# Optimization experiments

Hardware: AMD Instinct MI355X
Metric: run time of the kernel (lower is better)

## Reference

```python
import math
import jax, jax.numpy as jnp
import numpy as np

B, T, C, HS = 8, 2048, 1024, 64

def setup_inputs() -> dict:
    key = jax.random.key(0)
    kx, kq, kk, kv = jax.random.split(key, 4)
    x = jax.random.normal(kx, (B, T, C), dtype=jnp.float32)
    # match nn.Linear init scale roughly: U(-1/sqrt(C), 1/sqrt(C))
    lim = 1.0 / math.sqrt(C)
    Wq = jax.random.uniform(kq, (C, HS), minval=-lim, maxval=lim, dtype=jnp.float32)
    Wk = jax.random.uniform(kk, (C, HS), minval=-lim, maxval=lim, dtype=jnp.float32)
    Wv = jax.random.uniform(kv, (C, HS), minval=-lim, maxval=lim, dtype=jnp.float32)
    return {"x": x, "Wq": Wq, "Wk": Wk, "Wv": Wv}

def reference(x, Wq, Wk, Wv):
    # NOTE: original scales by 1/sqrt(hs) where hs = x.shape[-1] = embd_size,
    # not head_size. Faithfully reproduced.
    Tlen = x.shape[1]
    scale = 1.0 / math.sqrt(x.shape[-1])
    q = jnp.einsum('btc,ch->bth', x, Wq)
    k = jnp.einsum('btc,ch->bth', x, Wk)
    v = jnp.einsum('btc,ch->bth', x, Wv)
    wei = jnp.einsum('bth,bsh->bts', q, k) * scale  # [B,T,T]
    causal = jnp.tril(jnp.ones((Tlen, Tlen), dtype=bool))
    wei = jnp.where(causal, wei, -jnp.inf)
    wei = jax.nn.softmax(wei, axis=-1)
    # dropout p=0.0 -> identity
    out = jnp.einsum('bts,bsh->bth', wei, v)  # [B,T,HS]
    return out
```

## Files before the change

### kernel.cpp

```cpp
#include <hip/hip_runtime.h>
#include <hip/hip_bf16.h>


#define T_SEQ 2048
#define C_DIM 1024
#define HS 64
#define BT 16384

typedef short s8v __attribute__((ext_vector_type(8)));
typedef float f4v __attribute__((ext_vector_type(4)));

__device__ inline unsigned short f2bf(float f) {
  union { float f; unsigned u; } a; a.f = f;
  unsigned r = a.u + 0x7fffu + ((a.u >> 16) & 1u);
  return (unsigned short)(r >> 16);
}

__device__ inline unsigned pk2(float a, float b) {
  union { __hip_bfloat162 h; unsigned u; } c;
  c.h = __float22bfloat162_rn(make_float2(a, b));
  return c.u;
}

__device__ inline s8v cvt8(float4 v0, float4 v1) {
  union { unsigned u[4]; s8v v; } r;
  r.u[0] = pk2(v0.x, v0.y); r.u[1] = pk2(v0.z, v0.w);
  r.u[2] = pk2(v1.x, v1.y); r.u[3] = pk2(v1.z, v1.w);
  return r.v;
}

__device__ inline void gl_lds16(const void* g, unsigned char* lds_base,
                                unsigned uniform_byte_off) {
  __builtin_amdgcn_global_load_lds(
      (const __attribute__((address_space(1))) unsigned int*)g,
      (__attribute__((address_space(3))) unsigned int*)(lds_base + uniform_byte_off),
      16, 0, 0);
}

__global__ __launch_bounds__(256) void wt_kernel(
    const float* __restrict__ Wq, const float* __restrict__ Wk,
    const float* __restrict__ Wv, unsigned short* __restrict__ wt) {
  __shared__ float tile[64][65];
  const int bid = blockIdx.x;
  const int mat = bid >> 4, kt = bid & 15;
  const float* W = (mat == 0) ? Wq : ((mat == 1) ? Wk : Wv);
  const int t = threadIdx.x;
  const int n = t & 63, kr = t >> 6;
#pragma unroll
  for (int j = 0; j < 16; ++j) {
    const int kl = j * 4 + kr;
    tile[kl][n] = W[(kt * 64 + kl) * HS + n];
  }
  __syncthreads();
  const int n2 = t >> 2, kp = t & 3;
  unsigned int* orow =
      (unsigned int*)(wt + (size_t)(mat * 64 + n2) * C_DIM + kt * 64);
#pragma unroll
  for (int i = 0; i < 8; ++i) {
    const int k0 = kp * 16 + i * 2;
    unsigned int lo = f2bf(tile[k0][n2]);
    unsigned int hi = f2bf(tile[k0 + 1][n2]);
    orow[kp * 8 + i] = lo | (hi << 16);
  }
}

__global__ __launch_bounds__(256) void qkv_kernel(
    const float* __restrict__ x, const unsigned short* __restrict__ wt,
    unsigned short* __restrict__ qws, unsigned short* __restrict__ kws,
    unsigned short* __restrict__ vtws) {
  __shared__ unsigned char abuf[2][8192];
  __shared__ unsigned char bbuf[2][24576];

  const int tid  = threadIdx.x;
  const int wv   = tid >> 6;
  const int lane = tid & 63;
  const int m    = lane & 15;
  const int quad = lane >> 4;
  const int row0 = blockIdx.x * 32;
  const int mh   = wv >> 1;
  const int ng   = (wv & 1) * 6;

  f4v acc[6];
#pragma unroll
  for (int j = 0; j < 6; ++j) acc[j] = (f4v)0.0f;

  const unsigned au = (unsigned)__builtin_amdgcn_readfirstlane(tid & 192) << 4;

  const float* agp[2];
#pragma unroll
  for (int j = 0; j < 2; ++j) {
    const int s = tid + j * 256;
    const int r = s >> 4, p = (s & 15) ^ (r & 15);
    agp[j] = x + (size_t)(row0 + r) * C_DIM + p * 4;
  }
  const unsigned short* bgp[6];
#pragma unroll
  for (int j = 0; j < 6; ++j) {
    const int s = tid + j * 256;
    const int n = s >> 3, p = (s & 7) ^ (n & 7);
    bgp[j] = wt + (size_t)n * C_DIM + p * 8;
  }

  int aoff[2][2];
#pragma unroll
  for (int c = 0; c < 2; ++c)
#pragma unroll
    for (int t = 0; t < 2; ++t)
      aoff[c][t] = (((mh * 16 + m) * 16) + ((c * 8 + 2 * quad + t) ^ m)) << 4;
  int boff[6][2];
#pragma unroll
  for (int j = 0; j < 6; ++j) {
    const int n = (ng + j) * 16 + m;
#pragma unroll
    for (int c = 0; c < 2; ++c)
      boff[j][c] = (n * 8 + ((c * 4 + quad) ^ (n & 7))) << 4;
  }

#define STAGE(buf, kk)                                                       \
  do {                                                                       \
    _Pragma("unroll") for (int j = 0; j < 2; ++j)                            \
        gl_lds16(agp[j] + (kk), abuf[buf], au + (unsigned)(j * 4096));       \
    _Pragma("unroll") for (int j = 0; j < 6; ++j)                            \
        gl_lds16(bgp[j] + (kk), bbuf[buf], au + (unsigned)(j * 4096));       \
  } while (0)

  STAGE(0, 0);
  for (int it = 0; it < 16; ++it) {
    __syncthreads();
    if (it < 15) STAGE((it + 1) & 1, (it + 1) * 64);
    const unsigned char* aB = abuf[it & 1];
    const unsigned char* bB = bbuf[it & 1];
#pragma unroll
    for (int c = 0; c < 2; ++c) {
      float4 xa = *(const float4*)(aB + aoff[c][0]);
      float4 xb = *(const float4*)(aB + aoff[c][1]);
      s8v a = cvt8(xa, xb);
#pragma unroll
      for (int j = 0; j < 6; ++j) {
        s8v b = *(const s8v*)(bB + boff[j][c]);
        acc[j] = __builtin_amdgcn_mfma_f32_16x16x32_bf16(a, b, acc[j], 0, 0, 0);
      }
    }
  }
#undef STAGE

  const float qscale = 1.4426950408889634f / 32.0f;
#pragma unroll
  for (int j = 0; j < 6; ++j) {
    const int nt = ng + j;
    const int mat = nt >> 2, ct = nt & 3;
    const int col = ct * 16 + m;
#pragma unroll
    for (int r = 0; r < 4; ++r) {
      const int row = row0 + mh * 16 + quad * 4 + r;
      const float v = acc[j][r];
      if (mat == 0) {
        qws[row * HS + col] = f2bf(v * qscale);
      } else if (mat == 1) {
        kws[row * HS + col] = f2bf(v);
      } else {
        const int bb = row >> 11, t = row & 2047;
        const int tp = (t & ~63) | (((t & 15) << 2) | ((t >> 4) & 3));
        vtws[(bb * HS + col) * T_SEQ + tp] = f2bf(v);
      }
    }
  }
}

union __align__(16) AttnSh {
  unsigned short p[8][4][16 * 72];
  float mo[8][32][64];
};

__global__ __launch_bounds__(512) void attn_kernel(
    const unsigned short* __restrict__ qws, const unsigned short* __restrict__ kws,
    const unsigned short* __restrict__ vtws, float* __restrict__ out) {
  __shared__ AttnSh sh;
  __shared__ float ml[8][32];

  const int tid  = threadIdx.x;
  const int wv   = tid >> 6;
  const int lane = tid & 63;
  const int m    = lane & 15;
  const int quad = lane >> 4;
  const int b    = blockIdx.x & 7;
  const int pr   = blockIdx.x >> 3;
  const int rS   = pr * 32;
  const int rB   = (63 - pr) * 32;
  const int grS  = b * T_SEQ + rS;
  const int grB  = b * T_SEQ + rB;

  const unsigned short* qpS = qws + (size_t)(grS + m) * HS + quad * 8;
  const unsigned short* qpB = qws + (size_t)(grB + m) * HS + quad * 8;
  s8v aq[4][2];
  aq[0][0] = *(const s8v*)qpS;
  aq[0][1] = *(const s8v*)(qpS + 32);
  aq[1][0] = *(const s8v*)(qpS + 16 * HS);
  aq[1][1] = *(const s8v*)(qpS + 16 * HS + 32);
  aq[2][0] = *(const s8v*)qpB;
  aq[2][1] = *(const s8v*)(qpB + 32);
  aq[3][0] = *(const s8v*)(qpB + 16 * HS);
  aq[3][1] = *(const s8v*)(qpB + 16 * HS + 32);

  float li[4][4];
  f4v o[4][4];
#pragma unroll
  for (int t = 0; t < 4; ++t)
#pragma unroll
    for (int i = 0; i < 4; ++i) { li[t][i] = 0.f; o[t][i] = (f4v)0.0f; }

  const int nstS = (rS + 32 + 63) >> 6;
  const int nstB = (rB + 32 + 63) >> 6;
  const int qb0 = rS + quad * 4;
  const int qb1 = qb0 + 16;
  const int qb2 = rB + quad * 4;
  const int qb3 = qb2 + 16;
  const unsigned short* kbase = kws + (size_t)b * T_SEQ * HS;
  const unsigned short* vbase = vtws + (size_t)b * HS * T_SEQ;

#define QKT(t, qbase)                                                        \
  {                                                                          \
    f4v s_[4];                                                               \
    _Pragma("unroll") for (int ns = 0; ns < 4; ++ns) {                       \
      f4v u_ = (f4v)0.0f;                                                    \
      u_ = __builtin_amdgcn_mfma_f32_16x16x32_bf16(aq[t][0], kf[ns][0], u_, 0, 0, 0); \
      u_ = __builtin_amdgcn_mfma_f32_16x16x32_bf16(aq[t][1], kf[ns][1], u_, 0, 0, 0); \
      s_[ns] = u_;                                                           \
    }                                                                        \
    _Pragma("unroll") for (int r = 0; r < 4; ++r) {                          \
      const int qr = (qbase) + r;                                            \
      const float p0 = (sm      > qr) ? 0.f : __builtin_amdgcn_exp2f(s_[0][r]); \
      const float p1 = (sm + 16 > qr) ? 0.f : __builtin_amdgcn_exp2f(s_[1][r]); \
      const float p2 = (sm + 32 > qr) ? 0.f : __builtin_amdgcn_exp2f(s_[2][r]); \
      const float p3 = (sm + 48 > qr) ? 0.f : __builtin_amdgcn_exp2f(s_[3][r]); \
      li[t][r] += (p0 + p1) + (p2 + p3);                                     \
      *(uint2*)&sh.p[wv][t][(quad * 4 + r) * 72 + m * 4] =                   \
          make_uint2(pk2(p0, p1), pk2(p2, p3));                              \
    }                                                                        \
  }

#define PVT(t)                                                               \
  {                                                                          \
    const unsigned short* pl_ = sh.p[wv][t];                                 \
    s8v a0_ = *(const s8v*)&pl_[m * 72 + quad * 8];                          \
    s8v a1_ = *(const s8v*)&pl_[m * 72 + 32 + quad * 8];                     \
    _Pragma("unroll") for (int hn = 0; hn < 4; ++hn) {                       \
      o[t][hn] = __builtin_amdgcn_mfma_f32_16x16x32_bf16(a0_, vf[hn][0], o[t][hn], 0, 0, 0); \
      o[t][hn] = __builtin_amdgcn_mfma_f32_16x16x32_bf16(a1_, vf[hn][1], o[t][hn], 0, 0, 0); \
    }                                                                        \
  }

  for (int st = wv; st < nstB; st += 8) {
    const int s0 = st * 64;

    s8v kf[4][2];
#pragma unroll
    for (int ns = 0; ns < 4; ++ns) {
      const unsigned short* kp = &kbase[(size_t)(s0 + ns * 16 + m) * HS + quad * 8];
      kf[ns][0] = *(const s8v*)kp;
      kf[ns][1] = *(const s8v*)(kp + 32);
    }
    s8v vf[4][2];
#pragma unroll
    for (int hn = 0; hn < 4; ++hn) {
      const unsigned short* vp = &vbase[(size_t)(hn * 16 + m) * T_SEQ + s0 + quad * 8];
      vf[hn][0] = *(const s8v*)vp;
      vf[hn][1] = *(const s8v*)(vp + 32);
    }

    const int sm = s0 + m;
    const bool low = (st < nstS);
    if (low) { QKT(0, qb0); QKT(1, qb1); }
    QKT(2, qb2);
    QKT(3, qb3);
    if (low) { PVT(0); PVT(1); }
    PVT(2);
    PVT(3);
  }
#undef QKT
#undef PVT

#pragma unroll
  for (int t = 0; t < 4; ++t)
#pragma unroll
    for (int r = 0; r < 4; ++r) {
      float s = li[t][r];
      s += __shfl_xor(s, 1); s += __shfl_xor(s, 2);
      s += __shfl_xor(s, 4); s += __shfl_xor(s, 8);
      li[t][r] = s;
    }

  const int row = tid >> 4, c4 = (tid & 15) * 4;
#pragma unroll
  for (int ps = 0; ps < 2; ++ps) {
    __syncthreads();
#pragma unroll
    for (int hn = 0; hn < 4; ++hn)
#pragma unroll
      for (int r = 0; r < 4; ++r) {
        sh.mo[wv][quad * 4 + r][hn * 16 + m]      = o[2 * ps][hn][r];
        sh.mo[wv][16 + quad * 4 + r][hn * 16 + m] = o[2 * ps + 1][hn][r];
      }
    if (m == 0) {
#pragma unroll
      for (int r = 0; r < 4; ++r) {
        ml[wv][quad * 4 + r]      = li[2 * ps][r];
        ml[wv][16 + quad * 4 + r] = li[2 * ps + 1][r];
      }
    }
    __syncthreads();

    float ls = 0.f;
#pragma unroll
    for (int w = 0; w < 8; ++w) ls += ml[w][row];
    const float inv = 1.0f / ls;
    float ax = 0.f, ay = 0.f, az = 0.f, aw = 0.f;
#pragma unroll
    for (int w = 0; w < 8; ++w) {
      float4 v = *(const float4*)&sh.mo[w][row][c4];
      ax += v.x; ay += v.y; az += v.z; aw += v.w;
    }
    const int gr = ps ? grB : grS;
    float4 res;
    res.x = ax * inv; res.y = ay * inv; res.z = az * inv; res.w = aw * inv;
    *(float4*)&out[(size_t)(gr + row) * HS + c4] = res;
  }
}

extern "C" void kernel_launch(void* const* d_in, const int* in_sizes, int n_in,
                              void* d_out, int out_size, void* d_ws, size_t ws_size,
                              hipStream_t stream) {
  const float* x  = (const float*)d_in[0];
  const float* Wq = (const float*)d_in[1];
  const float* Wk = (const float*)d_in[2];
  const float* Wv = (const float*)d_in[3];
  float* out = (float*)d_out;

  unsigned short* qws  = (unsigned short*)d_ws;
  unsigned short* kws  = qws + (size_t)BT * HS;
  unsigned short* vtws = kws + (size_t)BT * HS;
  unsigned short* wt   = vtws + (size_t)BT * HS;

  wt_kernel<<<dim3(48), dim3(256), 0, stream>>>(Wq, Wk, Wv, wt);
  qkv_kernel<<<dim3(BT / 32), dim3(256), 0, stream>>>(x, wt, qws, kws, vtws);
  attn_kernel<<<dim3(256), dim3(512), 0, stream>>>(qws, kws, vtws, out);
}
```

Measured before the change: 135.4 us.

## Fuse weight transpose, QKV projection and attention into one cooperative kernel

Replaces the three separate launches (weight transpose/convert, QKV projection, attention) with a single cooperative kernel of 256 blocks that uses grid-wide syncs between the phases. The QKV phase is retiled to 64 rows per 512-thread block so the same grid shape serves every phase. The aim is to remove two kernel launch gaps and their tail drain. In exchange it adds grid.sync and threadfence overhead and a larger shared-memory union, and the QKV phase now runs only 256 blocks instead of 512.

```diff
diff --git a/kernel.cpp b/kernel.cpp
--- a/kernel.cpp
+++ b/kernel.cpp
@@ -1,5 +1,8 @@
 #include <hip/hip_runtime.h>
 #include <hip/hip_bf16.h>
+#include <hip/hip_cooperative_groups.h>
+
+namespace cg = cooperative_groups;
 
 
 #define T_SEQ 2048
@@ -37,186 +40,187 @@
       16, 0, 0);
 }
 
-__global__ __launch_bounds__(256) void wt_kernel(
-    const float* __restrict__ Wq, const float* __restrict__ Wk,
-    const float* __restrict__ Wv, unsigned short* __restrict__ wt) {
-  __shared__ float tile[64][65];
-  const int bid = blockIdx.x;
-  const int mat = bid >> 4, kt = bid & 15;
-  const float* W = (mat == 0) ? Wq : ((mat == 1) ? Wk : Wv);
-  const int t = threadIdx.x;
-  const int n = t & 63, kr = t >> 6;
-#pragma unroll
-  for (int j = 0; j < 16; ++j) {
-    const int kl = j * 4 + kr;
-    tile[kl][n] = W[(kt * 64 + kl) * HS + n];
-  }
-  __syncthreads();
-  const int n2 = t >> 2, kp = t & 3;
-  unsigned int* orow =
-      (unsigned int*)(wt + (size_t)(mat * 64 + n2) * C_DIM + kt * 64);
-#pragma unroll
-  for (int i = 0; i < 8; ++i) {
-    const int k0 = kp * 16 + i * 2;
-    unsigned int lo = f2bf(tile[k0][n2]);
-    unsigned int hi = f2bf(tile[k0 + 1][n2]);
-    orow[kp * 8 + i] = lo | (hi << 16);
-  }
-}
-
-__global__ __launch_bounds__(256) void qkv_kernel(
-    const float* __restrict__ x, const unsigned short* __restrict__ wt,
-    unsigned short* __restrict__ qws, unsigned short* __restrict__ kws,
-    unsigned short* __restrict__ vtws) {
-  __shared__ unsigned char abuf[2][8192];
-  __shared__ unsigned char bbuf[2][24576];
+union __align__(16) FusedSh {
+  struct { unsigned char a[2][16384]; unsigned char b[2][24576]; } qk;
+  struct { unsigned short p[8][4][16 * 72]; } at;
+  struct { float mo[8][32][64]; } mg;
+  float wtile[64][65];
+};
+
+__global__ __launch_bounds__(512, 2) void fused_kernel(
+    const float* __restrict__ x, const float* __restrict__ Wq,
+    const float* __restrict__ Wk, const float* __restrict__ Wv,
+    unsigned short* __restrict__ wt, unsigned short* __restrict__ qws,
+    unsigned short* __restrict__ kws, unsigned short* __restrict__ vtws,
+    float* __restrict__ out) {
+  __shared__ FusedSh sh;
+  __shared__ float ml[8][32];
+
+  cg::grid_group grid = cg::this_grid();
 
   const int tid  = threadIdx.x;
+  const int bid  = blockIdx.x;
   const int wv   = tid >> 6;
   const int lane = tid & 63;
   const int m    = lane & 15;
   const int quad = lane >> 4;
-  const int row0 = blockIdx.x * 32;
-  const int mh   = wv >> 1;
-  const int ng   = (wv & 1) * 6;
-
-  f4v acc[6];
-#pragma unroll
-  for (int j = 0; j < 6; ++j) acc[j] = (f4v)0.0f;
-
-  const unsigned au = (unsigned)__builtin_amdgcn_readfirstlane(tid & 192) << 4;
-
-  const float* agp[2];
-#pragma unroll
-  for (int j = 0; j < 2; ++j) {
-    const int s = tid + j * 256;
-    const int r = s >> 4, p = (s & 15) ^ (r & 15);
-    agp[j] = x + (size_t)(row0 + r) * C_DIM + p * 4;
-  }
-  const unsigned short* bgp[6];
-#pragma unroll
-  for (int j = 0; j < 6; ++j) {
-    const int s = tid + j * 256;
-    const int n = s >> 3, p = (s & 7) ^ (n & 7);
-    bgp[j] = wt + (size_t)n * C_DIM + p * 8;
-  }
-
-  int aoff[2][2];
-#pragma unroll
-  for (int c = 0; c < 2; ++c)
-#pragma unroll
-    for (int t = 0; t < 2; ++t)
-      aoff[c][t] = (((mh * 16 + m) * 16) + ((c * 8 + 2 * quad + t) ^ m)) << 4;
-  int boff[6][2];
-#pragma unroll
-  for (int j = 0; j < 6; ++j) {
-    const int n = (ng + j) * 16 + m;
+
+  if (bid < 48) {
+    const int mat = bid >> 4, kt = bid & 15;
+    const float* W = (mat == 0) ? Wq : ((mat == 1) ? Wk : Wv);
+    const int n = tid & 63, kr = tid >> 6;
+#pragma unroll
+    for (int j = 0; j < 8; ++j) {
+      const int kl = j * 8 + kr;
+      sh.wtile[kl][n] = W[(kt * 64 + kl) * HS + n];
+    }
+    __syncthreads();
+    const int n2 = tid >> 3, kp = tid & 7;
+    unsigned int* orow =
+        (unsigned int*)(wt + (size_t)(mat * 64 + n2) * C_DIM + kt * 64);
+#pragma unroll
+    for (int i = 0; i < 4; ++i) {
+      const int k0 = kp * 8 + i * 2;
+      unsigned lo = f2bf(sh.wtile[k0][n2]);
+      unsigned hi = f2bf(sh.wtile[k0 + 1][n2]);
+      orow[kp * 4 + i] = lo | (hi << 16);
+    }
+  }
+  __threadfence();
+  grid.sync();
+  __threadfence();
+
+  {
+    const int wq = wv & 3, th = wv >> 2;
+    const int mh = wq >> 1, ng = (wq & 1) * 6;
+    const int row0 = bid * 64;
+
+    f4v acc[6];
+#pragma unroll
+    for (int j = 0; j < 6; ++j) acc[j] = (f4v)0.0f;
+
+    const unsigned au = (unsigned)__builtin_amdgcn_readfirstlane(tid & 448) << 4;
+
+    const float* agp[2];
+#pragma unroll
+    for (int j = 0; j < 2; ++j) {
+      const int s = tid + j * 512;
+      const int r = s >> 4, p = (s & 15) ^ (r & 15);
+      agp[j] = x + (size_t)(row0 + r) * C_DIM + p * 4;
+    }
+    const unsigned short* bgp[3];
+#pragma unroll
+    for (int j = 0; j < 3; ++j) {
+      const int s = tid + j * 512;
+      const int n = s >> 3, p = (s & 7) ^ (n & 7);
+      bgp[j] = wt + (size_t)n * C_DIM + p * 8;
+    }
+
+    int aoff[2][2];
 #pragma unroll
     for (int c = 0; c < 2; ++c)
-      boff[j][c] = (n * 8 + ((c * 4 + quad) ^ (n & 7))) << 4;
-  }
+#pragma unroll
+      for (int t = 0; t < 2; ++t)
+        aoff[c][t] =
+            (((th * 32 + mh * 16 + m) * 16) + ((c * 8 + 2 * quad + t) ^ m)) << 4;
+    int boff[6][2];
+#pragma unroll
+    for (int j = 0; j < 6; ++j) {
+      const int n = (ng + j) * 16 + m;
+#pragma unroll
+      for (int c = 0; c < 2; ++c)
+        boff[j][c] = (n * 8 + ((c * 4 + quad) ^ (n & 7))) << 4;
+    }
 
 #define STAGE(buf, kk)                                                       \
   do {                                                                       \
     _Pragma("unroll") for (int j = 0; j < 2; ++j)                            \
-        gl_lds16(agp[j] + (kk), abuf[buf], au + (unsigned)(j * 4096));       \
-    _Pragma("unroll") for (int j = 0; j < 6; ++j)                            \
-        gl_lds16(bgp[j] + (kk), bbuf[buf], au + (unsigned)(j * 4096));       \
+        gl_lds16(agp[j] + (kk), sh.qk.a[buf], au + (unsigned)(j * 8192));    \
+    _Pragma("unroll") for (int j = 0; j < 3; ++j)                            \
+        gl_lds16(bgp[j] + (kk), sh.qk.b[buf], au + (unsigned)(j * 8192));    \
   } while (0)
 
-  STAGE(0, 0);
-  for (int it = 0; it < 16; ++it) {
-    __syncthreads();
-    if (it < 15) STAGE((it + 1) & 1, (it + 1) * 64);
-    const unsigned char* aB = abuf[it & 1];
-    const unsigned char* bB = bbuf[it & 1];
-#pragma unroll
-    for (int c = 0; c < 2; ++c) {
-      float4 xa = *(const float4*)(aB + aoff[c][0]);
-      float4 xb = *(const float4*)(aB + aoff[c][1]);
-      s8v a = cvt8(xa, xb);
-#pragma unroll
-      for (int j = 0; j < 6; ++j) {
-        s8v b = *(const s8v*)(bB + boff[j][c]);
-        acc[j] = __builtin_amdgcn_mfma_f32_16x16x32_bf16(a, b, acc[j], 0, 0, 0);
-      }
-    }
-  }
+    STAGE(0, 0);
+    for (int it = 0; it < 16; ++it) {
+      __syncthreads();
+      if (it < 15) STAGE((it + 1) & 1, (it + 1) * 64);
+      const unsigned char* aB = sh.qk.a[it & 1];
+      const unsigned char* bB = sh.qk.b[it & 1];
+#pragma unroll
+      for (int c = 0; c < 2; ++c) {
+        float4 xa = *(const float4*)(aB + aoff[c][0]);
+        float4 xb = *(const float4*)(aB + aoff[c][1]);
+        s8v a = cvt8(xa, xb);
+#pragma unroll
+        for (int j = 0; j < 6; ++j) {
+          s8v b = *(const s8v*)(bB + boff[j][c]);
+          acc[j] = __builtin_amdgcn_mfma_f32_16x16x32_bf16(a, b, acc[j], 0, 0, 0);
+        }
+      }
+    }
 #undef STAGE
 
-  const float qscale = 1.4426950408889634f / 32.0f;
-#pragma unroll
-  for (int j = 0; j < 6; ++j) {
-    const int nt = ng + j;
-    const int mat = nt >> 2, ct = nt & 3;
-    const int col = ct * 16 + m;
-#pragma unroll
-    for (int r = 0; r < 4; ++r) {
-      const int row = row0 + mh * 16 + quad * 4 + r;
-      const float v = acc[j][r];
-      if (mat == 0) {
-        qws[row * HS + col] = f2bf(v * qscale);
-      } else if (mat == 1) {
-        kws[row * HS + col] = f2bf(v);
-      } else {
-        const int bb = row >> 11, t = row & 2047;
-        const int tp = (t & ~63) | (((t & 15) << 2) | ((t >> 4) & 3));
-        vtws[(bb * HS + col) * T_SEQ + tp] = f2bf(v);
-      }
-    }
-  }
-}
-
-union __align__(16) AttnSh {
-  unsigned short p[8][4][16 * 72];
-  float mo[8][32][64];
-};
-
-__global__ __launch_bounds__(512) void attn_kernel(
-    const unsigned short* __restrict__ qws, const unsigned short* __restrict__ kws,
-    const unsigned short* __restrict__ vtws, float* __restrict__ out) {
-  __shared__ AttnSh sh;
-  __shared__ float ml[8][32];
-
-  const int tid  = threadIdx.x;
-  const int wv   = tid >> 6;
-  const int lane = tid & 63;
-  const int m    = lane & 15;
-  const int quad = lane >> 4;
-  const int b    = blockIdx.x & 7;
-  const int pr   = blockIdx.x >> 3;
-  const int rS   = pr * 32;
-  const int rB   = (63 - pr) * 32;
-  const int grS  = b * T_SEQ + rS;
-  const int grB  = b * T_SEQ + rB;
-
-  const unsigned short* qpS = qws + (size_t)(grS + m) * HS + quad * 8;
-  const unsigned short* qpB = qws + (size_t)(grB + m) * HS + quad * 8;
-  s8v aq[4][2];
-  aq[0][0] = *(const s8v*)qpS;
-  aq[0][1] = *(const s8v*)(qpS + 32);
-  aq[1][0] = *(const s8v*)(qpS + 16 * HS);
-  aq[1][1] = *(const s8v*)(qpS + 16 * HS + 32);
-  aq[2][0] = *(const s8v*)qpB;
-  aq[2][1] = *(const s8v*)(qpB + 32);
-  aq[3][0] = *(const s8v*)(qpB + 16 * HS);
-  aq[3][1] = *(const s8v*)(qpB + 16 * HS + 32);
-
-  float li[4][4];
-  f4v o[4][4];
-#pragma unroll
-  for (int t = 0; t < 4; ++t)
-#pragma unroll
-    for (int i = 0; i < 4; ++i) { li[t][i] = 0.f; o[t][i] = (f4v)0.0f; }
-
-  const int nstS = (rS + 32 + 63) >> 6;
-  const int nstB = (rB + 32 + 63) >> 6;
-  const int qb0 = rS + quad * 4;
-  const int qb1 = qb0 + 16;
-  const int qb2 = rB + quad * 4;
-  const int qb3 = qb2 + 16;
-  const unsigned short* kbase = kws + (size_t)b * T_SEQ * HS;
-  const unsigned short* vbase = vtws + (size_t)b * HS * T_SEQ;
+    const float qscale = 1.4426950408889634f / 32.0f;
+#pragma unroll
+    for (int j = 0; j < 6; ++j) {
+      const int nt = ng + j;
+      const int mat = nt >> 2, ct = nt & 3;
+      const int col = ct * 16 + m;
+#pragma unroll
+      for (int r = 0; r < 4; ++r) {
+        const int row = row0 + th * 32 + mh * 16 + quad * 4 + r;
+        const float v = acc[j][r];
+        if (mat == 0) {
+          qws[row * HS + col] = f2bf(v * qscale);
+        } else if (mat == 1) {
+          kws[row * HS + col] = f2bf(v);
+        } else {
+          const int bb = row >> 11, t = row & 2047;
+          const int tp = (t & ~63) | (((t & 15) << 2) | ((t >> 4) & 3));
+          vtws[(bb * HS + col) * T_SEQ + tp] = f2bf(v);
+        }
+      }
+    }
+  }
+  __threadfence();
+  grid.sync();
+  __threadfence();
+
+  {
+    const int b  = bid & 7;
+    const int pr = bid >> 3;
+    const int rS = pr * 32;
+    const int rB = (63 - pr) * 32;
+    const int grS = b * T_SEQ + rS;
+    const int grB = b * T_SEQ + rB;
+
+    const unsigned short* qpS = qws + (size_t)(grS + m) * HS + quad * 8;
+    const unsigned short* qpB = qws + (size_t)(grB + m) * HS + quad * 8;
+    s8v aq[4][2];
+    aq[0][0] = *(const s8v*)qpS;
+    aq[0][1] = *(const s8v*)(qpS + 32);
+    aq[1][0] = *(const s8v*)(qpS + 16 * HS);
+    aq[1][1] = *(const s8v*)(qpS + 16 * HS + 32);
+    aq[2][0] = *(const s8v*)qpB;
+    aq[2][1] = *(const s8v*)(qpB + 32);
+    aq[3][0] = *(const s8v*)(qpB + 16 * HS);
+    aq[3][1] = *(const s8v*)(qpB + 16 * HS + 32);
+
+    float li[4][4];
+    f4v o[4][4];
+#pragma unroll
+    for (int t = 0; t < 4; ++t)
+#pragma unroll
+      for (int i = 0; i < 4; ++i) { li[t][i] = 0.f; o[t][i] = (f4v)0.0f; }
+
+    const int nstS = (rS + 32 + 63) >> 6;
+    const int nstB = (rB + 32 + 63) >> 6;
+    const int qb0 = rS + quad * 4;
+    const int qb1 = qb0 + 16;
+    const int qb2 = rB + quad * 4;
+    const int qb3 = qb2 + 16;
+    const unsigned short* kbase = kws + (size_t)b * T_SEQ * HS;
+    const unsigned short* vbase = vtws + (size_t)b * HS * T_SEQ;
 
 #define QKT(t, qbase)                                                        \
   {                                                                          \
@@ -234,14 +238,14 @@
       const float p2 = (sm + 32 > qr) ? 0.f : __builtin_amdgcn_exp2f(s_[2][r]); \
       const float p3 = (sm + 48 > qr) ? 0.f : __builtin_amdgcn_exp2f(s_[3][r]); \
       li[t][r] += (p0 + p1) + (p2 + p3);                                     \
-      *(uint2*)&sh.p[wv][t][(quad * 4 + r) * 72 + m * 4] =                   \
+      *(uint2*)&sh.at.p[wv][t][(quad * 4 + r) * 72 + m * 4] =                \
           make_uint2(pk2(p0, p1), pk2(p2, p3));                              \
     }                                                                        \
   }
 
 #define PVT(t)                                                               \
   {                                                                          \
-    const unsigned short* pl_ = sh.p[wv][t];                                 \
+    const unsigned short* pl_ = sh.at.p[wv][t];                              \
     s8v a0_ = *(const s8v*)&pl_[m * 72 + quad * 8];                          \
     s8v a1_ = *(const s8v*)&pl_[m * 72 + 32 + quad * 8];                     \
     _Pragma("unroll") for (int hn = 0; hn < 4; ++hn) {                       \
@@ -250,80 +254,81 @@
     }                                                                        \
   }
 
-  for (int st = wv; st < nstB; st += 8) {
-    const int s0 = st * 64;
-
-    s8v kf[4][2];
-#pragma unroll
-    for (int ns = 0; ns < 4; ++ns) {
-      const unsigned short* kp = &kbase[(size_t)(s0 + ns * 16 + m) * HS + quad * 8];
-      kf[ns][0] = *(const s8v*)kp;
-      kf[ns][1] = *(const s8v*)(kp + 32);
-    }
-    s8v vf[4][2];
-#pragma unroll
-    for (int hn = 0; hn < 4; ++hn) {
-      const unsigned short* vp = &vbase[(size_t)(hn * 16 + m) * T_SEQ + s0 + quad * 8];
-      vf[hn][0] = *(const s8v*)vp;
-      vf[hn][1] = *(const s8v*)(vp + 32);
-    }
-
-    const int sm = s0 + m;
-    const bool low = (st < nstS);
-    if (low) { QKT(0, qb0); QKT(1, qb1); }
-    QKT(2, qb2);
-    QKT(3, qb3);
-    if (low) { PVT(0); PVT(1); }
-    PVT(2);
-    PVT(3);
-  }
+    for (int st = wv; st < nstB; st += 8) {
+      const int s0 = st * 64;
+
+      s8v kf[4][2];
+#pragma unroll
+      for (int ns = 0; ns < 4; ++ns) {
+        const unsigned short* kp = &kbase[(size_t)(s0 + ns * 16 + m) * HS + quad * 8];
+        kf[ns][0] = *(const s8v*)kp;
+        kf[ns][1] = *(const s8v*)(kp + 32);
+      }
+      s8v vf[4][2];
+#pragma unroll
+      for (int hn = 0; hn < 4; ++hn) {
+        const unsigned short* vp = &vbase[(size_t)(hn * 16 + m) * T_SEQ + s0 + quad * 8];
+        vf[hn][0] = *(const s8v*)vp;
+        vf[hn][1] = *(const s8v*)(vp + 32);
+      }
+
+      const int sm = s0 + m;
+      const bool low = (st < nstS);
+      if (low) { QKT(0, qb0); QKT(1, qb1); }
+      QKT(2, qb2);
+      QKT(3, qb3);
+      if (low) { PVT(0); PVT(1); }
+      PVT(2);
+      PVT(3);
+    }
 #undef QKT
 #undef PVT
 
 #pragma unroll
-  for (int t = 0; t < 4; ++t)
-#pragma unroll
-    for (int r = 0; r < 4; ++r) {
-      float s = li[t][r];
-      s += __shfl_xor(s, 1); s += __shfl_xor(s, 2);
-      s += __shfl_xor(s, 4); s += __shfl_xor(s, 8);
-      li[t][r] = s;
-    }
-
-  const int row = tid >> 4, c4 = (tid & 15) * 4;
-#pragma unroll
-  for (int ps = 0; ps < 2; ++ps) {
-    __syncthreads();
-#pragma unroll
-    for (int hn = 0; hn < 4; ++hn)
+    for (int t = 0; t < 4; ++t)
 #pragma unroll
       for (int r = 0; r < 4; ++r) {
-        sh.mo[wv][quad * 4 + r][hn * 16 + m]      = o[2 * ps][hn][r];
-        sh.mo[wv][16 + quad * 4 + r][hn * 16 + m] = o[2 * ps + 1][hn][r];
-      }
-    if (m == 0) {
-#pragma unroll
-      for (int r = 0; r < 4; ++r) {
-        ml[wv][quad * 4 + r]      = li[2 * ps][r];
-        ml[wv][16 + quad * 4 + r] = li[2 * ps + 1][r];
-      }
-    }
-    __syncthreads();
-
-    float ls = 0.f;
-#pragma unroll
-    for (int w = 0; w < 8; ++w) ls += ml[w][row];
-    const float inv = 1.0f / ls;
-    float ax = 0.f, ay = 0.f, az = 0.f, aw = 0.f;
-#pragma unroll
-    for (int w = 0; w < 8; ++w) {
-      float4 v = *(const float4*)&sh.mo[w][row][c4];
-      ax += v.x; ay += v.y; az += v.z; aw += v.w;
-    }
-    const int gr = ps ? grB : grS;
-    float4 res;
-    res.x = ax * inv; res.y = ay * inv; res.z = az * inv; res.w = aw * inv;
-    *(float4*)&out[(size_t)(gr + row) * HS + c4] = res;
+        float s = li[t][r];
+        s += __shfl_xor(s, 1); s += __shfl_xor(s, 2);
+        s += __shfl_xor(s, 4); s += __shfl_xor(s, 8);
+        li[t][r] = s;
+      }
+
+    const int row = tid >> 4, c4 = (tid & 15) * 4;
+#pragma unroll
+    for (int ps = 0; ps < 2; ++ps) {
+      __syncthreads();
+#pragma unroll
+      for (int hn = 0; hn < 4; ++hn)
+#pragma unroll
+        for (int r = 0; r < 4; ++r) {
+          sh.mg.mo[wv][quad * 4 + r][hn * 16 + m]      = o[2 * ps][hn][r];
+          sh.mg.mo[wv][16 + quad * 4 + r][hn * 16 + m] = o[2 * ps + 1][hn][r];
+        }
+      if (m == 0) {
+#pragma unroll
+        for (int r = 0; r < 4; ++r) {
+          ml[wv][quad * 4 + r]      = li[2 * ps][r];
+          ml[wv][16 + quad * 4 + r] = li[2 * ps + 1][r];
+        }
+      }
+      __syncthreads();
+
+      float ls = 0.f;
+#pragma unroll
+      for (int w = 0; w < 8; ++w) ls += ml[w][row];
+      const float inv = 1.0f / ls;
+      float ax = 0.f, ay = 0.f, az = 0.f, aw = 0.f;
+#pragma unroll
+      for (int w = 0; w < 8; ++w) {
+        float4 v = *(const float4*)&sh.mg.mo[w][row][c4];
+        ax += v.x; ay += v.y; az += v.z; aw += v.w;
+      }
+      const int gr = ps ? grB : grS;
+      float4 res;
+      res.x = ax * inv; res.y = ay * inv; res.z = az * inv; res.w = aw * inv;
+      *(float4*)&out[(size_t)(gr + row) * HS + c4] = res;
+    }
   }
 }
 
@@ -341,7 +346,9 @@
   unsigned short* vtws = kws + (size_t)BT * HS;
   unsigned short* wt   = vtws + (size_t)BT * HS;
 
-  wt_kernel<<<dim3(48), dim3(256), 0, stream>>>(Wq, Wk, Wv, wt);
-  qkv_kernel<<<dim3(BT / 32), dim3(256), 0, stream>>>(x, wt, qws, kws, vtws);
-  attn_kernel<<<dim3(256), dim3(512), 0, stream>>>(qws, kws, vtws, out);
-}
+  void* args[] = {(void*)&x, (void*)&Wq, (void*)&Wk, (void*)&Wv,
+                  (void*)&wt, (void*)&qws, (void*)&kws, (void*)&vtws,
+                  (void*)&out};
+  hipLaunchCooperativeKernel((void*)fused_kernel, dim3(256), dim3(512),
+                             args, 0, stream);
+}
```

Result: slower. 388.8 us (+187.1%).

## Keep softmax probabilities in registers via transposed QK^T and grow QKV tiles

Applied to the files above, without the earlier changes.

The attention kernel now computes S^T by swapping the MFMA operands, so each lane holds probabilities along the key dimension. It packs them straight into bf16 A-operands for the PV MFMA, which removes the LDS round-trip for P, and the V workspace permutation is changed to match the new key ordering. Row sums now need only two cross-quad shuffles. Separately, the QKV projection block grows to 64 rows with 512 threads, so each weight tile staged in LDS is shared by twice as many rows, at the cost of more LDS per block and fewer resident blocks.

```diff
diff --git a/kernel.cpp b/kernel.cpp
--- a/kernel.cpp
+++ b/kernel.cpp
@@ -64,11 +64,11 @@
   }
 }
 
-__global__ __launch_bounds__(256) void qkv_kernel(
+__global__ __launch_bounds__(512) void qkv_kernel(
     const float* __restrict__ x, const unsigned short* __restrict__ wt,
     unsigned short* __restrict__ qws, unsigned short* __restrict__ kws,
     unsigned short* __restrict__ vtws) {
-  __shared__ unsigned char abuf[2][8192];
+  __shared__ unsigned char abuf[2][16384];
   __shared__ unsigned char bbuf[2][24576];
 
   const int tid  = threadIdx.x;
@@ -76,27 +76,27 @@
   const int lane = tid & 63;
   const int m    = lane & 15;
   const int quad = lane >> 4;
-  const int row0 = blockIdx.x * 32;
-  const int mh   = wv >> 1;
-  const int ng   = (wv & 1) * 6;
+  const int wq = wv & 3, th = wv >> 2;
+  const int mh = wq >> 1, ng = (wq & 1) * 6;
+  const int row0 = blockIdx.x * 64;
 
   f4v acc[6];
 #pragma unroll
   for (int j = 0; j < 6; ++j) acc[j] = (f4v)0.0f;
 
-  const unsigned au = (unsigned)__builtin_amdgcn_readfirstlane(tid & 192) << 4;
+  const unsigned au = (unsigned)__builtin_amdgcn_readfirstlane(tid & 448) << 4;
 
   const float* agp[2];
 #pragma unroll
   for (int j = 0; j < 2; ++j) {
-    const int s = tid + j * 256;
+    const int s = tid + j * 512;
     const int r = s >> 4, p = (s & 15) ^ (r & 15);
     agp[j] = x + (size_t)(row0 + r) * C_DIM + p * 4;
   }
-  const unsigned short* bgp[6];
-#pragma unroll
-  for (int j = 0; j < 6; ++j) {
-    const int s = tid + j * 256;
+  const unsigned short* bgp[3];
+#pragma unroll
+  for (int j = 0; j < 3; ++j) {
+    const int s = tid + j * 512;
     const int n = s >> 3, p = (s & 7) ^ (n & 7);
     bgp[j] = wt + (size_t)n * C_DIM + p * 8;
   }
@@ -106,7 +106,8 @@
   for (int c = 0; c < 2; ++c)
 #pragma unroll
     for (int t = 0; t < 2; ++t)
-      aoff[c][t] = (((mh * 16 + m) * 16) + ((c * 8 + 2 * quad + t) ^ m)) << 4;
+      aoff[c][t] =
+          (((th * 32 + mh * 16 + m) * 16) + ((c * 8 + 2 * quad + t) ^ m)) << 4;
   int boff[6][2];
 #pragma unroll
   for (int j = 0; j < 6; ++j) {
@@ -119,9 +120,9 @@
 #define STAGE(buf, kk)                                                       \
   do {                                                                       \
     _Pragma("unroll") for (int j = 0; j < 2; ++j)                            \
-        gl_lds16(agp[j] + (kk), abuf[buf], au + (unsigned)(j * 4096));       \
-    _Pragma("unroll") for (int j = 0; j < 6; ++j)                            \
-        gl_lds16(bgp[j] + (kk), bbuf[buf], au + (unsigned)(j * 4096));       \
+        gl_lds16(agp[j] + (kk), abuf[buf], au + (unsigned)(j * 8192));       \
+    _Pragma("unroll") for (int j = 0; j < 3; ++j)                            \
+        gl_lds16(bgp[j] + (kk), bbuf[buf], au + (unsigned)(j * 8192));       \
   } while (0)
 
   STAGE(0, 0);
@@ -152,7 +153,7 @@
     const int col = ct * 16 + m;
 #pragma unroll
     for (int r = 0; r < 4; ++r) {
-      const int row = row0 + mh * 16 + quad * 4 + r;
+      const int row = row0 + th * 32 + mh * 16 + quad * 4 + r;
       const float v = acc[j][r];
       if (mat == 0) {
         qws[row * HS + col] = f2bf(v * qscale);
@@ -160,22 +161,18 @@
         kws[row * HS + col] = f2bf(v);
       } else {
         const int bb = row >> 11, t = row & 2047;
-        const int tp = (t & ~63) | (((t & 15) << 2) | ((t >> 4) & 3));
-        vtws[(bb * HS + col) * T_SEQ + tp] = f2bf(v);
+        const int s = t & 63;
+        const int jp = (s & 32) | ((s & 12) << 1) | ((s & 16) >> 2) | (s & 3);
+        vtws[(bb * HS + col) * T_SEQ + ((t & ~63) | jp)] = f2bf(v);
       }
     }
   }
 }
-
-union __align__(16) AttnSh {
-  unsigned short p[8][4][16 * 72];
-  float mo[8][32][64];
-};
 
 __global__ __launch_bounds__(512) void attn_kernel(
     const unsigned short* __restrict__ qws, const unsigned short* __restrict__ kws,
     const unsigned short* __restrict__ vtws, float* __restrict__ out) {
-  __shared__ AttnSh sh;
+  __shared__ float mo[8][32][64];
   __shared__ float ml[8][32];
 
   const int tid  = threadIdx.x;
@@ -202,51 +199,50 @@
   aq[3][0] = *(const s8v*)(qpB + 16 * HS);
   aq[3][1] = *(const s8v*)(qpB + 16 * HS + 32);
 
-  float li[4][4];
+  float li[4] = {0.f, 0.f, 0.f, 0.f};
   f4v o[4][4];
 #pragma unroll
   for (int t = 0; t < 4; ++t)
 #pragma unroll
-    for (int i = 0; i < 4; ++i) { li[t][i] = 0.f; o[t][i] = (f4v)0.0f; }
+    for (int i = 0; i < 4; ++i) o[t][i] = (f4v)0.0f;
 
   const int nstS = (rS + 32 + 63) >> 6;
   const int nstB = (rB + 32 + 63) >> 6;
-  const int qb0 = rS + quad * 4;
-  const int qb1 = qb0 + 16;
-  const int qb2 = rB + quad * 4;
-  const int qb3 = qb2 + 16;
+  const int qb0 = rS;
+  const int qb1 = rS + 16;
+  const int qb2 = rB;
+  const int qb3 = rB + 16;
   const unsigned short* kbase = kws + (size_t)b * T_SEQ * HS;
   const unsigned short* vbase = vtws + (size_t)b * HS * T_SEQ;
 
-#define QKT(t, qbase)                                                        \
+#define TILE(t, qb)                                                          \
   {                                                                          \
     f4v s_[4];                                                               \
     _Pragma("unroll") for (int ns = 0; ns < 4; ++ns) {                       \
       f4v u_ = (f4v)0.0f;                                                    \
-      u_ = __builtin_amdgcn_mfma_f32_16x16x32_bf16(aq[t][0], kf[ns][0], u_, 0, 0, 0); \
-      u_ = __builtin_amdgcn_mfma_f32_16x16x32_bf16(aq[t][1], kf[ns][1], u_, 0, 0, 0); \
+      u_ = __builtin_amdgcn_mfma_f32_16x16x32_bf16(kf[ns][0], aq[t][0], u_, 0, 0, 0); \
+      u_ = __builtin_amdgcn_mfma_f32_16x16x32_bf16(kf[ns][1], aq[t][1], u_, 0, 0, 0); \
       s_[ns] = u_;                                                           \
     }                                                                        \
-    _Pragma("unroll") for (int r = 0; r < 4; ++r) {                          \
-      const int qr = (qbase) + r;                                            \
-      const float p0 = (sm      > qr) ? 0.f : __builtin_amdgcn_exp2f(s_[0][r]); \
-      const float p1 = (sm + 16 > qr) ? 0.f : __builtin_amdgcn_exp2f(s_[1][r]); \
-      const float p2 = (sm + 32 > qr) ? 0.f : __builtin_amdgcn_exp2f(s_[2][r]); \
-      const float p3 = (sm + 48 > qr) ? 0.f : __builtin_amdgcn_exp2f(s_[3][r]); \
-      li[t][r] += (p0 + p1) + (p2 + p3);                                     \
-      *(uint2*)&sh.p[wv][t][(quad * 4 + r) * 72 + m * 4] =                   \
-          make_uint2(pk2(p0, p1), pk2(p2, p3));                              \
+    const int qr_ = (qb) + m;                                                \
+    union { unsigned u[4]; s8v v; } paA_, paB_;                              \
+    _Pragma("unroll") for (int ns = 0; ns < 4; ++ns) {                       \
+      const int sb_ = s0 + ns * 16 + quad * 4;                               \
+      const float p0 = (sb_     > qr_) ? 0.f : __builtin_amdgcn_exp2f(s_[ns][0]); \
+      const float p1 = (sb_ + 1 > qr_) ? 0.f : __builtin_amdgcn_exp2f(s_[ns][1]); \
+      const float p2 = (sb_ + 2 > qr_) ? 0.f : __builtin_amdgcn_exp2f(s_[ns][2]); \
+      const float p3 = (sb_ + 3 > qr_) ? 0.f : __builtin_amdgcn_exp2f(s_[ns][3]); \
+      li[t] += (p0 + p1) + (p2 + p3);                                        \
+      if (ns < 2) {                                                          \
+        paA_.u[ns * 2] = pk2(p0, p1); paA_.u[ns * 2 + 1] = pk2(p2, p3);      \
+      } else {                                                               \
+        paB_.u[(ns - 2) * 2] = pk2(p0, p1);                                  \
+        paB_.u[(ns - 2) * 2 + 1] = pk2(p2, p3);                              \
+      }                                                                      \
     }                                                                        \
-  }
-
-#define PVT(t)                                                               \
-  {                                                                          \
-    const unsigned short* pl_ = sh.p[wv][t];                                 \
-    s8v a0_ = *(const s8v*)&pl_[m * 72 + quad * 8];                          \
-    s8v a1_ = *(const s8v*)&pl_[m * 72 + 32 + quad * 8];                     \
     _Pragma("unroll") for (int hn = 0; hn < 4; ++hn) {                       \
-      o[t][hn] = __builtin_amdgcn_mfma_f32_16x16x32_bf16(a0_, vf[hn][0], o[t][hn], 0, 0, 0); \
-      o[t][hn] = __builtin_amdgcn_mfma_f32_16x16x32_bf16(a1_, vf[hn][1], o[t][hn], 0, 0, 0); \
+      o[t][hn] = __builtin_amdgcn_mfma_f32_16x16x32_bf16(paA_.v, vf[hn][0], o[t][hn], 0, 0, 0); \
+      o[t][hn] = __builtin_amdgcn_mfma_f32_16x16x32_bf16(paB_.v, vf[hn][1], o[t][hn], 0, 0, 0); \
     }                                                                        \
   }
 
@@ -268,27 +264,19 @@
       vf[hn][1] = *(const s8v*)(vp + 32);
     }
 
-    const int sm = s0 + m;
     const bool low = (st < nstS);
-    if (low) { QKT(0, qb0); QKT(1, qb1); }
-    QKT(2, qb2);
-    QKT(3, qb3);
-    if (low) { PVT(0); PVT(1); }
-    PVT(2);
-    PVT(3);
-  }
-#undef QKT
-#undef PVT
-
-#pragma unroll
-  for (int t = 0; t < 4; ++t)
-#pragma unroll
-    for (int r = 0; r < 4; ++r) {
-      float s = li[t][r];
-      s += __shfl_xor(s, 1); s += __shfl_xor(s, 2);
-      s += __shfl_xor(s, 4); s += __shfl_xor(s, 8);
-      li[t][r] = s;
-    }
+    if (low) { TILE(0, qb0); TILE(1, qb1); }
+    TILE(2, qb2);
+    TILE(3, qb3);
+  }
+#undef TILE
+
+#pragma unroll
+  for (int t = 0; t < 4; ++t) {
+    float s = li[t];
+    s += __shfl_xor(s, 16); s += __shfl_xor(s, 32);
+    li[t] = s;
+  }
 
   const int row = tid >> 4, c4 = (tid & 15) * 4;
 #pragma unroll
@@ -298,15 +286,12 @@
     for (int hn = 0; hn < 4; ++hn)
 #pragma unroll
       for (int r = 0; r < 4; ++r) {
-        sh.mo[wv][quad * 4 + r][hn * 16 + m]      = o[2 * ps][hn][r];
-        sh.mo[wv][16 + quad * 4 + r][hn * 16 + m] = o[2 * ps + 1][hn][r];
+        mo[wv][quad * 4 + r][hn * 16 + m]      = o[2 * ps][hn][r];
+        mo[wv][16 + quad * 4 + r][hn * 16 + m] = o[2 * ps + 1][hn][r];
       }
-    if (m == 0) {
-#pragma unroll
-      for (int r = 0; r < 4; ++r) {
-        ml[wv][quad * 4 + r]      = li[2 * ps][r];
-        ml[wv][16 + quad * 4 + r] = li[2 * ps + 1][r];
-      }
+    if (quad == 0) {
+      ml[wv][m]      = li[2 * ps];
+      ml[wv][16 + m] = li[2 * ps + 1];
     }
     __syncthreads();
 
@@ -317,7 +302,7 @@
     float ax = 0.f, ay = 0.f, az = 0.f, aw = 0.f;
 #pragma unroll
     for (int w = 0; w < 8; ++w) {
-      float4 v = *(const float4*)&sh.mo[w][row][c4];
+      float4 v = *(const float4*)&mo[w][row][c4];
       ax += v.x; ay += v.y; az += v.z; aw += v.w;
     }
     const int gr = ps ? grB : grS;
@@ -342,6 +327,6 @@
   unsigned short* wt   = vtws + (size_t)BT * HS;
 
   wt_kernel<<<dim3(48), dim3(256), 0, stream>>>(Wq, Wk, Wv, wt);
-  qkv_kernel<<<dim3(BT / 32), dim3(256), 0, stream>>>(x, wt, qws, kws, vtws);
+  qkv_kernel<<<dim3(BT / 64), dim3(512), 0, stream>>>(x, wt, qws, kws, vtws);
   attn_kernel<<<dim3(256), dim3(512), 0, stream>>>(qws, kws, vtws, out);
 }
```

New measurement: 133.3 us. Within noise of the previous version (-1.6%).
